# Performance work log

Hardware: AMD Instinct MI355X
Metric: run time of the kernel (lower is better)

The kernel has to match this reference:

```python
import jax, jax.numpy as jnp
import numpy as np

H = 2048            # hidden_size
INTER = 8192        # intermediate_size
E = 16              # num_experts
V = 32000           # vocab_size
I = INTER // E      # per-expert intermediate (tp_size=1) = 512
N = 4096            # num_tokens
BASE_ROUTING_SCALE = 10.0


def setup_inputs() -> dict:
    key = jax.random.key(0)
    ks = jax.random.split(key, 6)
    x = jax.random.normal(ks[0], (N, H), dtype=jnp.float32)
    token_ids = jax.random.randint(ks[1], (N,), 0, V)
    mu = jax.random.normal(ks[2], (N, H), dtype=jnp.float32)
    # kaiming-uniform-ish scaled params
    gate_up_proj = jax.random.normal(ks[3], (E, H, 2 * I), dtype=jnp.float32) * (1.0 / np.sqrt(H))
    down_proj = jax.random.normal(ks[4], (E, I, H), dtype=jnp.float32) * (1.0 / np.sqrt(I))
    # mu_router initialized to zeros in the module; use small random so routing is actually mu-biased
    mu_router_w = jax.random.normal(ks[5], (E, H), dtype=jnp.float32) * 0.02
    return {"x": x, "token_ids": token_ids, "mu": mu,
            "gate_up_proj": gate_up_proj, "down_proj": down_proj,
            "mu_router_w": mu_router_w}


def reference(x, token_ids, mu, gate_up_proj, down_proj, mu_router_w):
    # --- routing: expert = token_id % E, biased by mu logits ---
    base = jnp.clip(token_ids, 0, V - 1) % E              # [N]
    logits = (jax.nn.one_hot(base, E, dtype=jnp.float32) * BASE_ROUTING_SCALE
              + mu @ mu_router_w.T)                       # [N, E]
    expert_ids = jnp.argmax(logits, axis=-1)              # [N]

    Iloc = gate_up_proj.shape[-1] // 2

    # --- grouped expert SwiGLU MLP: scan over experts, mask-combine outputs ---
    def step(acc, inp):
        wg, wd, e = inp
        gu = x @ wg                                       # [N, 2I]
        h = jax.nn.silu(gu[:, :Iloc]) * gu[:, Iloc:]      # [N, I]
        o = h @ wd                                        # [N, H]
        acc = acc + jnp.where((expert_ids == e)[:, None], o, 0.0)
        return acc, None

    out0 = jnp.zeros_like(x)
    out, _ = jax.lax.scan(step, out0, (gate_up_proj, down_proj, jnp.arange(E)))
    return out
```

## Files before the change

### kernel.cpp

```cpp
#include <hip/hip_runtime.h>
#include <hip/hip_bf16.h>

#define NT 4096
#define HD 2048
#define NE 16
#define ID 512
#define TWO_I 1024
#define PITCH 72
#define MAXITEMS 47

typedef __attribute__((ext_vector_type(8))) short bf16x8_t;
typedef __attribute__((ext_vector_type(4))) float f32x4_t;

__device__ __forceinline__ unsigned short f2bf(float f) {
  union { float f; unsigned int u; } v; v.f = f;
  unsigned int r = v.u + 0x7fffu + ((v.u >> 16) & 1u);
  return (unsigned short)(r >> 16);
}

__global__ void k_cast_x(const float* __restrict__ x, unsigned short* __restrict__ xb) {
  size_t i = ((size_t)blockIdx.x * 256 + threadIdx.x) * 8;
  float4 a = *(const float4*)(x + i);
  float4 b = *(const float4*)(x + i + 4);
  unsigned int w0 = (unsigned)f2bf(a.x) | ((unsigned)f2bf(a.y) << 16);
  unsigned int w1 = (unsigned)f2bf(a.z) | ((unsigned)f2bf(a.w) << 16);
  unsigned int w2 = (unsigned)f2bf(b.x) | ((unsigned)f2bf(b.y) << 16);
  unsigned int w3 = (unsigned)f2bf(b.z) | ((unsigned)f2bf(b.w) << 16);
  uint4 pk; pk.x = w0; pk.y = w1; pk.z = w2; pk.w = w3;
  *(uint4*)(xb + i) = pk;
}

__global__ void k_route(const float* __restrict__ mu, const int* __restrict__ tok,
                        const float* __restrict__ wr, int* __restrict__ eid) {
  int t = blockIdx.x;
  int tid = threadIdx.x;
  float p[NE];
#pragma unroll
  for (int e = 0; e < NE; ++e) p[e] = 0.f;
  const float* m = mu + (size_t)t * HD;
  for (int h = tid; h < HD; h += 256) {
    float mv = m[h];
#pragma unroll
    for (int e = 0; e < NE; ++e) p[e] += mv * wr[e * HD + h];
  }
#pragma unroll
  for (int e = 0; e < NE; ++e) {
    float v = p[e];
#pragma unroll
    for (int s = 32; s; s >>= 1) v += __shfl_xor(v, s, 64);
    p[e] = v;
  }
  __shared__ float red[4][NE];
  int lane = tid & 63, wv = tid >> 6;
  if (lane == 0) {
#pragma unroll
    for (int e = 0; e < NE; ++e) red[wv][e] = p[e];
  }
  __syncthreads();
  if (tid == 0) {
    int tk = tok[t];
    if (tk < 0) tk = 0;
    if (tk > 31999) tk = 31999;
    int base = tk & 15;
    float best = -3.0e38f; int bi = 0;
    for (int e = 0; e < NE; ++e) {
      float v = red[0][e] + red[1][e] + red[2][e] + red[3][e];
      if (e == base) v += 10.0f;
      if (v > best) { best = v; bi = e; }
    }
    eid[t] = bi;
  }
}

__global__ void k_init(int* counts, int* cursors) {
  int i = threadIdx.x;
  if (i < NE) { counts[i] = 0; cursors[i] = 0; }
}
__global__ void k_hist(const int* __restrict__ eid, int* __restrict__ counts) {
  int t = blockIdx.x * 256 + threadIdx.x;
  if (t < NT) atomicAdd(&counts[eid[t]], 1);
}
__global__ void k_scan(const int* __restrict__ counts, int* __restrict__ offsets,
                       int* __restrict__ cursors, int* __restrict__ wk) {
  if (threadIdx.x == 0) {
    int s = 0;
    for (int e = 0; e < NE; ++e) { offsets[e] = s; cursors[e] = s; s += counts[e]; }
    offsets[NE] = s;
    int n = 0;
    for (int e = 0; e < NE; ++e) {
      int tiles = (counts[e] + 127) >> 7;
      for (int m = 0; m < tiles; ++m) { wk[n++] = e | (m << 8); }
    }
    wk[MAXITEMS] = n;
  }
}
__global__ void k_scatter(const int* __restrict__ eid, int* __restrict__ cursors,
                          int* __restrict__ tlist) {
  int t = blockIdx.x * 256 + threadIdx.x;
  if (t < NT) {
    int e = eid[t];
    int pos = atomicAdd(&cursors[e], 1);
    tlist[pos] = t;
  }
}

__global__ __launch_bounds__(256, 3) void k_gemm1(
    const unsigned short* __restrict__ xb, const float* __restrict__ gup,
    const int* __restrict__ offsets, const int* __restrict__ tlist,
    const int* __restrict__ wk, unsigned short* __restrict__ hbuf) {
  int item = blockIdx.y;
  if (item >= wk[MAXITEMS]) return;
  int w = wk[item];
  int e = w & 255, tb = (w >> 8) * 128;
  int off = offsets[e], cnt = offsets[e + 1] - off;
  int c0 = blockIdx.x * 32;

  __shared__ unsigned short lA[128 * PITCH];
  __shared__ unsigned short lB[64 * PITCH];
  __shared__ int ltok[128];

  int tid = threadIdx.x, lane = tid & 63, wv = tid >> 6;
  if (tid < 128) {
    int r = tb + tid; if (r > cnt - 1) r = cnt - 1;
    ltok[tid] = tlist[off + r];
  }
  __syncthreads();

  const float* Wg = gup + (size_t)e * HD * TWO_I;

  const unsigned short* aP[4];
  unsigned aL[4];
#pragma unroll
  for (int it = 0; it < 4; ++it) {
    int id = tid + 256 * it;
    int row = id >> 3, oct = id & 7;
    aP[it] = xb + (size_t)ltok[row] * HD + oct * 8;
    aL[it] = row * PITCH + oct * 8;
  }
  const float* bP[2];
  unsigned bL[2];
#pragma unroll
  for (int it = 0; it < 2; ++it) {
    int id = tid + 256 * it;
    int col = id & 31, grp = (id >> 5) & 1, koct = id >> 6;
    int gcol = grp ? (ID + c0 + col) : (c0 + col);
    bP[it] = Wg + (size_t)koct * 8 * TWO_I + gcol;
    bL[it] = (grp * 32 + col) * PITCH + koct * 8;
  }

  f32x4_t zero = {0.f, 0.f, 0.f, 0.f};
  f32x4_t accg[2][2], accu[2][2];
#pragma unroll
  for (int m = 0; m < 2; ++m)
#pragma unroll
    for (int n = 0; n < 2; ++n) { accg[m][n] = zero; accu[m][n] = zero; }

  for (int kt = 0; kt < 32; ++kt) {
    uint4 a0 = *(const uint4*)aP[0], a1 = *(const uint4*)aP[1];
    uint4 a2 = *(const uint4*)aP[2], a3 = *(const uint4*)aP[3];
    float b0[8], b1[8];
#pragma unroll
    for (int j = 0; j < 8; ++j) b0[j] = bP[0][(size_t)j * TWO_I];
#pragma unroll
    for (int j = 0; j < 8; ++j) b1[j] = bP[1][(size_t)j * TWO_I];
#pragma unroll
    for (int it = 0; it < 4; ++it) aP[it] += 64;
#pragma unroll
    for (int it = 0; it < 2; ++it) bP[it] += (size_t)64 * TWO_I;

    __syncthreads();
    *(uint4*)&lA[aL[0]] = a0; *(uint4*)&lA[aL[1]] = a1;
    *(uint4*)&lA[aL[2]] = a2; *(uint4*)&lA[aL[3]] = a3;
    uint4 p0, p1;
    p0.x = (unsigned)f2bf(b0[0]) | ((unsigned)f2bf(b0[1]) << 16);
    p0.y = (unsigned)f2bf(b0[2]) | ((unsigned)f2bf(b0[3]) << 16);
    p0.z = (unsigned)f2bf(b0[4]) | ((unsigned)f2bf(b0[5]) << 16);
    p0.w = (unsigned)f2bf(b0[6]) | ((unsigned)f2bf(b0[7]) << 16);
    p1.x = (unsigned)f2bf(b1[0]) | ((unsigned)f2bf(b1[1]) << 16);
    p1.y = (unsigned)f2bf(b1[2]) | ((unsigned)f2bf(b1[3]) << 16);
    p1.z = (unsigned)f2bf(b1[4]) | ((unsigned)f2bf(b1[5]) << 16);
    p1.w = (unsigned)f2bf(b1[6]) | ((unsigned)f2bf(b1[7]) << 16);
    *(uint4*)&lB[bL[0]] = p0; *(uint4*)&lB[bL[1]] = p1;
    __syncthreads();

    int mb = wv * 32, lr = lane & 15;
#pragma unroll
    for (int kk = 0; kk < 2; ++kk) {
      int klo = kk * 32 + 8 * (lane >> 4);
      bf16x8_t a[2], bg[2], bu[2];
#pragma unroll
      for (int m = 0; m < 2; ++m) a[m] = *(bf16x8_t*)&lA[(mb + m * 16 + lr) * PITCH + klo];
#pragma unroll
      for (int n = 0; n < 2; ++n) {
        bg[n] = *(bf16x8_t*)&lB[(n * 16 + lr) * PITCH + klo];
        bu[n] = *(bf16x8_t*)&lB[((32 + n * 16) + lr) * PITCH + klo];
      }
#pragma unroll
      for (int m = 0; m < 2; ++m)
#pragma unroll
        for (int n = 0; n < 2; ++n) {
          accg[m][n] = __builtin_amdgcn_mfma_f32_16x16x32_bf16(a[m], bg[n], accg[m][n], 0, 0, 0);
          accu[m][n] = __builtin_amdgcn_mfma_f32_16x16x32_bf16(a[m], bu[n], accu[m][n], 0, 0, 0);
        }
    }
  }

  int mb = wv * 32, lr = lane & 15, rq = (lane >> 4) * 4;
#pragma unroll
  for (int m = 0; m < 2; ++m)
#pragma unroll
    for (int n = 0; n < 2; ++n)
#pragma unroll
      for (int j = 0; j < 4; ++j) {
        int r = tb + mb + m * 16 + rq + j;
        if (r < cnt) {
          float g = accg[m][n][j], u = accu[m][n][j];
          float hv = (g / (1.f + __expf(-g))) * u;
          hbuf[(size_t)(off + r) * ID + c0 + n * 16 + lr] = f2bf(hv);
        }
      }
}

__global__ __launch_bounds__(256, 3) void k_gemm2(
    const unsigned short* __restrict__ hbuf, const float* __restrict__ dwn,
    const int* __restrict__ offsets, const int* __restrict__ tlist,
    const int* __restrict__ wk, float* __restrict__ out) {
  int item = blockIdx.y;
  if (item >= wk[MAXITEMS]) return;
  int w = wk[item];
  int e = w & 255, tb = (w >> 8) * 128;
  int off = offsets[e], cnt = offsets[e + 1] - off;
  int c0 = blockIdx.x * 64;

  __shared__ unsigned short lA[128 * PITCH];
  __shared__ unsigned short lB[64 * PITCH];

  int tid = threadIdx.x, lane = tid & 63, wv = tid >> 6;

  const float* Wd = dwn + (size_t)e * ID * HD;

  const unsigned short* aP[4];
  unsigned aL[4];
#pragma unroll
  for (int it = 0; it < 4; ++it) {
    int id = tid + 256 * it;
    int row = id >> 3, oct = id & 7;
    int r = tb + row; if (r > cnt - 1) r = cnt - 1;
    aP[it] = hbuf + (size_t)(off + r) * ID + oct * 8;
    aL[it] = row * PITCH + oct * 8;
  }
  const float* bP[2];
  unsigned bL[2];
#pragma unroll
  for (int it = 0; it < 2; ++it) {
    int id = tid + 256 * it;
    int col = id & 63, koct = id >> 6;
    bP[it] = Wd + (size_t)koct * 8 * HD + c0 + col;
    bL[it] = col * PITCH + koct * 8;
  }

  f32x4_t zero = {0.f, 0.f, 0.f, 0.f};
  f32x4_t acc[2][4];
#pragma unroll
  for (int m = 0; m < 2; ++m)
#pragma unroll
    for (int n = 0; n < 4; ++n) acc[m][n] = zero;

  for (int kt = 0; kt < 8; ++kt) {
    uint4 a0 = *(const uint4*)aP[0], a1 = *(const uint4*)aP[1];
    uint4 a2 = *(const uint4*)aP[2], a3 = *(const uint4*)aP[3];
    float b0[8], b1[8];
#pragma unroll
    for (int j = 0; j < 8; ++j) b0[j] = bP[0][(size_t)j * HD];
#pragma unroll
    for (int j = 0; j < 8; ++j) b1[j] = bP[1][(size_t)j * HD];
#pragma unroll
    for (int it = 0; it < 4; ++it) aP[it] += 64;
#pragma unroll
    for (int it = 0; it < 2; ++it) bP[it] += (size_t)64 * HD;

    __syncthreads();
    *(uint4*)&lA[aL[0]] = a0; *(uint4*)&lA[aL[1]] = a1;
    *(uint4*)&lA[aL[2]] = a2; *(uint4*)&lA[aL[3]] = a3;
    uint4 p0, p1;
    p0.x = (unsigned)f2bf(b0[0]) | ((unsigned)f2bf(b0[1]) << 16);
    p0.y = (unsigned)f2bf(b0[2]) | ((unsigned)f2bf(b0[3]) << 16);
    p0.z = (unsigned)f2bf(b0[4]) | ((unsigned)f2bf(b0[5]) << 16);
    p0.w = (unsigned)f2bf(b0[6]) | ((unsigned)f2bf(b0[7]) << 16);
    p1.x = (unsigned)f2bf(b1[0]) | ((unsigned)f2bf(b1[1]) << 16);
    p1.y = (unsigned)f2bf(b1[2]) | ((unsigned)f2bf(b1[3]) << 16);
    p1.z = (unsigned)f2bf(b1[4]) | ((unsigned)f2bf(b1[5]) << 16);
    p1.w = (unsigned)f2bf(b1[6]) | ((unsigned)f2bf(b1[7]) << 16);
    *(uint4*)&lB[bL[0]] = p0; *(uint4*)&lB[bL[1]] = p1;
    __syncthreads();

    int mb = wv * 32, lr = lane & 15;
#pragma unroll
    for (int kk = 0; kk < 2; ++kk) {
      int klo = kk * 32 + 8 * (lane >> 4);
      bf16x8_t a[2], b[4];
#pragma unroll
      for (int m = 0; m < 2; ++m) a[m] = *(bf16x8_t*)&lA[(mb + m * 16 + lr) * PITCH + klo];
#pragma unroll
      for (int n = 0; n < 4; ++n) b[n] = *(bf16x8_t*)&lB[(n * 16 + lr) * PITCH + klo];
#pragma unroll
      for (int m = 0; m < 2; ++m)
#pragma unroll
        for (int n = 0; n < 4; ++n)
          acc[m][n] = __builtin_amdgcn_mfma_f32_16x16x32_bf16(a[m], b[n], acc[m][n], 0, 0, 0);
    }
  }

  int mb = wv * 32, lr = lane & 15, rq = (lane >> 4) * 4;
#pragma unroll
  for (int m = 0; m < 2; ++m)
#pragma unroll
    for (int n = 0; n < 4; ++n)
#pragma unroll
      for (int j = 0; j < 4; ++j) {
        int r = tb + mb + m * 16 + rq + j;
        if (r < cnt) {
          out[(size_t)tlist[off + r] * HD + c0 + n * 16 + lr] = acc[m][n][j];
        }
      }
}

extern "C" void kernel_launch(void* const* d_in, const int* in_sizes, int n_in,
                              void* d_out, int out_size, void* d_ws, size_t ws_size,
                              hipStream_t stream) {
  (void)in_sizes; (void)n_in; (void)out_size; (void)ws_size;
  const float* x   = (const float*)d_in[0];
  const int*   tok = (const int*)d_in[1];
  const float* mu  = (const float*)d_in[2];
  const float* gup = (const float*)d_in[3];
  const float* dwn = (const float*)d_in[4];
  const float* wr  = (const float*)d_in[5];
  float* out = (float*)d_out;

  char* ws = (char*)d_ws;
  int* eid     = (int*)ws;
  int* tlist   = (int*)(ws + 16384);
  int* counts  = (int*)(ws + 32768);
  int* offsets = (int*)(ws + 32896);
  int* cursors = (int*)(ws + 33024);
  int* wk      = (int*)(ws + 33152);
  unsigned short* xb   = (unsigned short*)(ws + 65536);
  unsigned short* hbuf = (unsigned short*)(ws + 65536 + (size_t)NT * HD * 2);

  k_cast_x <<<4096, 256, 0, stream>>>(x, xb);
  k_route  <<<NT, 256, 0, stream>>>(mu, tok, wr, eid);
  k_init   <<<1, 64, 0, stream>>>(counts, cursors);
  k_hist   <<<16, 256, 0, stream>>>(eid, counts);
  k_scan   <<<1, 64, 0, stream>>>(counts, offsets, cursors, wk);
  k_scatter<<<16, 256, 0, stream>>>(eid, cursors, tlist);
  k_gemm1  <<<dim3(16, MAXITEMS), 256, 0, stream>>>(xb, gup, offsets, tlist, wk, hbuf);
  k_gemm2  <<<dim3(32, MAXITEMS), 256, 0, stream>>>(hbuf, dwn, offsets, tlist, wk, out);
}
```

Baseline: 188.3 us.

## Double-buffer GEMM tiles with direct global-to-LDS loads and swizzled A layout

Both expert GEMM kernels now stage A (bf16 activations) and B (fp32 weights) tiles straight from global memory into LDS using global_load_lds, double-buffered so the next K-tile is fetched while the current one is computed. The fp32 weight tile is converted to bf16 in an LDS-to-LDS pass into a padded transpose buffer, and the A tile uses an XOR swizzle instead of padding to avoid bank conflicts. This targets global-load latency and register staging in the main loop. In exchange it uses much more LDS, so launch bounds drop from 3 to 2 blocks per CU, and it adds an extra barrier and conversion pass per iteration.

```diff
diff --git a/kernel.cpp b/kernel.cpp
--- a/kernel.cpp
+++ b/kernel.cpp
@@ -17,16 +17,22 @@
   unsigned int r = v.u + 0x7fffu + ((v.u >> 16) & 1u);
   return (unsigned short)(r >> 16);
 }
+__device__ __forceinline__ unsigned pk2(unsigned short a, unsigned short b) {
+  return (unsigned)a | ((unsigned)b << 16);
+}
+__device__ __forceinline__ void gl_lds16(const void* g, void* l) {
+  __builtin_amdgcn_global_load_lds(
+      (const __attribute__((address_space(1))) unsigned int*)g,
+      (__attribute__((address_space(3))) unsigned int*)l, 16, 0, 0);
+}
 
 __global__ void k_cast_x(const float* __restrict__ x, unsigned short* __restrict__ xb) {
   size_t i = ((size_t)blockIdx.x * 256 + threadIdx.x) * 8;
   float4 a = *(const float4*)(x + i);
   float4 b = *(const float4*)(x + i + 4);
-  unsigned int w0 = (unsigned)f2bf(a.x) | ((unsigned)f2bf(a.y) << 16);
-  unsigned int w1 = (unsigned)f2bf(a.z) | ((unsigned)f2bf(a.w) << 16);
-  unsigned int w2 = (unsigned)f2bf(b.x) | ((unsigned)f2bf(b.y) << 16);
-  unsigned int w3 = (unsigned)f2bf(b.z) | ((unsigned)f2bf(b.w) << 16);
-  uint4 pk; pk.x = w0; pk.y = w1; pk.z = w2; pk.w = w3;
+  uint4 pk;
+  pk.x = pk2(f2bf(a.x), f2bf(a.y)); pk.y = pk2(f2bf(a.z), f2bf(a.w));
+  pk.z = pk2(f2bf(b.x), f2bf(b.y)); pk.w = pk2(f2bf(b.z), f2bf(b.w));
   *(uint4*)(xb + i) = pk;
 }
 
@@ -104,7 +110,7 @@
   }
 }
 
-__global__ __launch_bounds__(256, 3) void k_gemm1(
+__global__ __launch_bounds__(256, 2) void k_gemm1(
     const unsigned short* __restrict__ xb, const float* __restrict__ gup,
     const int* __restrict__ offsets, const int* __restrict__ tlist,
     const int* __restrict__ wk, unsigned short* __restrict__ hbuf) {
@@ -115,38 +121,46 @@
   int off = offsets[e], cnt = offsets[e + 1] - off;
   int c0 = blockIdx.x * 32;
 
-  __shared__ unsigned short lA[128 * PITCH];
-  __shared__ unsigned short lB[64 * PITCH];
+  __shared__ unsigned short Abuf[2][128 * 64];
+  __shared__ float Bbuf[2][64 * 64];
+  __shared__ unsigned short Pbuf[64 * PITCH];
   __shared__ int ltok[128];
 
   int tid = threadIdx.x, lane = tid & 63, wv = tid >> 6;
-  if (tid < 128) {
-    int r = tb + tid; if (r > cnt - 1) r = cnt - 1;
-    ltok[tid] = tlist[off + r];
-  }
+  if (tid < 128) { int r = tb + tid; if (r > cnt - 1) r = cnt - 1; ltok[tid] = tlist[off + r]; }
   __syncthreads();
 
-  const float* Wg = gup + (size_t)e * HD * TWO_I;
-
-  const unsigned short* aP[4];
-  unsigned aL[4];
-#pragma unroll
-  for (int it = 0; it < 4; ++it) {
-    int id = tid + 256 * it;
-    int row = id >> 3, oct = id & 7;
-    aP[it] = xb + (size_t)ltok[row] * HD + oct * 8;
-    aL[it] = row * PITCH + oct * 8;
-  }
-  const float* bP[2];
-  unsigned bL[2];
-#pragma unroll
-  for (int it = 0; it < 2; ++it) {
-    int id = tid + 256 * it;
-    int col = id & 31, grp = (id >> 5) & 1, koct = id >> 6;
-    int gcol = grp ? (ID + c0 + col) : (c0 + col);
-    bP[it] = Wg + (size_t)koct * 8 * TWO_I + gcol;
-    bL[it] = (grp * 32 + col) * PITCH + koct * 8;
-  }
+  const unsigned short* aSrc[4];
+  int aDst[4];
+  int cswz = (lane & 7) ^ ((lane >> 3) & 7);
+#pragma unroll
+  for (int i = 0; i < 4; ++i) {
+    int r = wv * 32 + i * 8 + (lane >> 3);
+    aSrc[i] = xb + (size_t)ltok[r] * HD + cswz * 8;
+    aDst[i] = (wv * 32 + i * 8) * 64;
+  }
+  const float* bSrc[4];
+  int bDst[4];
+  {
+    int cc = lane & 15;
+    int gcol = (cc < 8) ? (c0 + cc * 4) : (ID + c0 + (cc - 8) * 4);
+    const float* Wg = gup + (size_t)e * HD * TWO_I;
+#pragma unroll
+    for (int i = 0; i < 4; ++i) {
+      int kr = wv * 16 + i * 4 + (lane >> 4);
+      bSrc[i] = Wg + (size_t)kr * TWO_I + gcol;
+      bDst[i] = (wv * 16 + i * 4) * 64;
+    }
+  }
+
+  auto stage = [&](int buf) {
+#pragma unroll
+    for (int i = 0; i < 4; ++i) { gl_lds16(aSrc[i], &Abuf[buf][aDst[i]]); aSrc[i] += 64; }
+#pragma unroll
+    for (int i = 0; i < 4; ++i) { gl_lds16(bSrc[i], &Bbuf[buf][bDst[i]]); bSrc[i] += (size_t)64 * TWO_I; }
+  };
+
+  stage(0);
 
   f32x4_t zero = {0.f, 0.f, 0.f, 0.f};
   f32x4_t accg[2][2], accu[2][2];
@@ -155,45 +169,50 @@
 #pragma unroll
     for (int n = 0; n < 2; ++n) { accg[m][n] = zero; accu[m][n] = zero; }
 
+  int lr = lane & 15, hi = lane >> 4, mb = wv * 32;
+
   for (int kt = 0; kt < 32; ++kt) {
-    uint4 a0 = *(const uint4*)aP[0], a1 = *(const uint4*)aP[1];
-    uint4 a2 = *(const uint4*)aP[2], a3 = *(const uint4*)aP[3];
-    float b0[8], b1[8];
-#pragma unroll
-    for (int j = 0; j < 8; ++j) b0[j] = bP[0][(size_t)j * TWO_I];
-#pragma unroll
-    for (int j = 0; j < 8; ++j) b1[j] = bP[1][(size_t)j * TWO_I];
-#pragma unroll
-    for (int it = 0; it < 4; ++it) aP[it] += 64;
-#pragma unroll
-    for (int it = 0; it < 2; ++it) bP[it] += (size_t)64 * TWO_I;
-
-    __syncthreads();
-    *(uint4*)&lA[aL[0]] = a0; *(uint4*)&lA[aL[1]] = a1;
-    *(uint4*)&lA[aL[2]] = a2; *(uint4*)&lA[aL[3]] = a3;
-    uint4 p0, p1;
-    p0.x = (unsigned)f2bf(b0[0]) | ((unsigned)f2bf(b0[1]) << 16);
-    p0.y = (unsigned)f2bf(b0[2]) | ((unsigned)f2bf(b0[3]) << 16);
-    p0.z = (unsigned)f2bf(b0[4]) | ((unsigned)f2bf(b0[5]) << 16);
-    p0.w = (unsigned)f2bf(b0[6]) | ((unsigned)f2bf(b0[7]) << 16);
-    p1.x = (unsigned)f2bf(b1[0]) | ((unsigned)f2bf(b1[1]) << 16);
-    p1.y = (unsigned)f2bf(b1[2]) | ((unsigned)f2bf(b1[3]) << 16);
-    p1.z = (unsigned)f2bf(b1[4]) | ((unsigned)f2bf(b1[5]) << 16);
-    p1.w = (unsigned)f2bf(b1[6]) | ((unsigned)f2bf(b1[7]) << 16);
-    *(uint4*)&lB[bL[0]] = p0; *(uint4*)&lB[bL[1]] = p1;
-    __syncthreads();
-
-    int mb = wv * 32, lr = lane & 15;
+    int cur = kt & 1;
+    if (kt < 31) {
+      stage(cur ^ 1);
+      asm volatile("s_waitcnt vmcnt(8)" ::: "memory");
+    } else {
+      asm volatile("s_waitcnt vmcnt(0)" ::: "memory");
+    }
+    __builtin_amdgcn_sched_barrier(0);
+    __builtin_amdgcn_s_barrier();
+
+    {
+      int c = lane, ks = wv;
+      unsigned short tmp[16];
+#pragma unroll
+      for (int j = 0; j < 16; ++j) tmp[j] = f2bf(Bbuf[cur][(ks * 16 + j) * 64 + c]);
+      uint4 p0, p1;
+      p0.x = pk2(tmp[0], tmp[1]);   p0.y = pk2(tmp[2], tmp[3]);
+      p0.z = pk2(tmp[4], tmp[5]);   p0.w = pk2(tmp[6], tmp[7]);
+      p1.x = pk2(tmp[8], tmp[9]);   p1.y = pk2(tmp[10], tmp[11]);
+      p1.z = pk2(tmp[12], tmp[13]); p1.w = pk2(tmp[14], tmp[15]);
+      *(uint4*)&Pbuf[c * PITCH + ks * 16] = p0;
+      *(uint4*)&Pbuf[c * PITCH + ks * 16 + 8] = p1;
+    }
+    asm volatile("s_waitcnt lgkmcnt(0)" ::: "memory");
+    __builtin_amdgcn_sched_barrier(0);
+    __builtin_amdgcn_s_barrier();
+
 #pragma unroll
     for (int kk = 0; kk < 2; ++kk) {
-      int klo = kk * 32 + 8 * (lane >> 4);
+      int klo = kk * 32 + hi * 8;
       bf16x8_t a[2], bg[2], bu[2];
 #pragma unroll
-      for (int m = 0; m < 2; ++m) a[m] = *(bf16x8_t*)&lA[(mb + m * 16 + lr) * PITCH + klo];
+      for (int m = 0; m < 2; ++m) {
+        int R = mb + m * 16 + lr;
+        int ch = (kk * 4 + hi) ^ (R & 7);
+        a[m] = *(bf16x8_t*)&Abuf[cur][R * 64 + ch * 8];
+      }
 #pragma unroll
       for (int n = 0; n < 2; ++n) {
-        bg[n] = *(bf16x8_t*)&lB[(n * 16 + lr) * PITCH + klo];
-        bu[n] = *(bf16x8_t*)&lB[((32 + n * 16) + lr) * PITCH + klo];
+        bg[n] = *(bf16x8_t*)&Pbuf[(n * 16 + lr) * PITCH + klo];
+        bu[n] = *(bf16x8_t*)&Pbuf[(32 + n * 16 + lr) * PITCH + klo];
       }
 #pragma unroll
       for (int m = 0; m < 2; ++m)
@@ -203,9 +222,10 @@
           accu[m][n] = __builtin_amdgcn_mfma_f32_16x16x32_bf16(a[m], bu[n], accu[m][n], 0, 0, 0);
         }
     }
-  }
-
-  int mb = wv * 32, lr = lane & 15, rq = (lane >> 4) * 4;
+    if (kt < 31) __builtin_amdgcn_s_barrier();
+  }
+
+  int rq = hi * 4;
 #pragma unroll
   for (int m = 0; m < 2; ++m)
 #pragma unroll
@@ -221,7 +241,7 @@
       }
 }
 
-__global__ __launch_bounds__(256, 3) void k_gemm2(
+__global__ __launch_bounds__(256, 2) void k_gemm2(
     const unsigned short* __restrict__ hbuf, const float* __restrict__ dwn,
     const int* __restrict__ offsets, const int* __restrict__ tlist,
     const int* __restrict__ wk, float* __restrict__ out) {
@@ -232,32 +252,43 @@
   int off = offsets[e], cnt = offsets[e + 1] - off;
   int c0 = blockIdx.x * 64;
 
-  __shared__ unsigned short lA[128 * PITCH];
-  __shared__ unsigned short lB[64 * PITCH];
+  __shared__ unsigned short Abuf[2][128 * 64];
+  __shared__ float Bbuf[2][64 * 64];
+  __shared__ unsigned short Pbuf[64 * PITCH];
 
   int tid = threadIdx.x, lane = tid & 63, wv = tid >> 6;
 
-  const float* Wd = dwn + (size_t)e * ID * HD;
-
-  const unsigned short* aP[4];
-  unsigned aL[4];
-#pragma unroll
-  for (int it = 0; it < 4; ++it) {
-    int id = tid + 256 * it;
-    int row = id >> 3, oct = id & 7;
-    int r = tb + row; if (r > cnt - 1) r = cnt - 1;
-    aP[it] = hbuf + (size_t)(off + r) * ID + oct * 8;
-    aL[it] = row * PITCH + oct * 8;
-  }
-  const float* bP[2];
-  unsigned bL[2];
-#pragma unroll
-  for (int it = 0; it < 2; ++it) {
-    int id = tid + 256 * it;
-    int col = id & 63, koct = id >> 6;
-    bP[it] = Wd + (size_t)koct * 8 * HD + c0 + col;
-    bL[it] = col * PITCH + koct * 8;
-  }
+  const unsigned short* aSrc[4];
+  int aDst[4];
+  int cswz = (lane & 7) ^ ((lane >> 3) & 7);
+#pragma unroll
+  for (int i = 0; i < 4; ++i) {
+    int r = tb + wv * 32 + i * 8 + (lane >> 3);
+    if (r > cnt - 1) r = cnt - 1;
+    aSrc[i] = hbuf + (size_t)(off + r) * ID + cswz * 8;
+    aDst[i] = (wv * 32 + i * 8) * 64;
+  }
+  const float* bSrc[4];
+  int bDst[4];
+  {
+    int cc = lane & 15;
+    const float* Wd = dwn + (size_t)e * ID * HD;
+#pragma unroll
+    for (int i = 0; i < 4; ++i) {
+      int kr = wv * 16 + i * 4 + (lane >> 4);
+      bSrc[i] = Wd + (size_t)kr * HD + c0 + cc * 4;
+      bDst[i] = (wv * 16 + i * 4) * 64;
+    }
+  }
+
+  auto stage = [&](int buf) {
+#pragma unroll
+    for (int i = 0; i < 4; ++i) { gl_lds16(aSrc[i], &Abuf[buf][aDst[i]]); aSrc[i] += 64; }
+#pragma unroll
+    for (int i = 0; i < 4; ++i) { gl_lds16(bSrc[i], &Bbuf[buf][bDst[i]]); bSrc[i] += (size_t)64 * HD; }
+  };
+
+  stage(0);
 
   f32x4_t zero = {0.f, 0.f, 0.f, 0.f};
   f32x4_t acc[2][4];
@@ -266,52 +297,58 @@
 #pragma unroll
     for (int n = 0; n < 4; ++n) acc[m][n] = zero;
 
+  int lr = lane & 15, hi = lane >> 4, mb = wv * 32;
+
   for (int kt = 0; kt < 8; ++kt) {
-    uint4 a0 = *(const uint4*)aP[0], a1 = *(const uint4*)aP[1];
-    uint4 a2 = *(const uint4*)aP[2], a3 = *(const uint4*)aP[3];
-    float b0[8], b1[8];
-#pragma unroll
-    for (int j = 0; j < 8; ++j) b0[j] = bP[0][(size_t)j * HD];
-#pragma unroll
-    for (int j = 0; j < 8; ++j) b1[j] = bP[1][(size_t)j * HD];
-#pragma unroll
-    for (int it = 0; it < 4; ++it) aP[it] += 64;
-#pragma unroll
-    for (int it = 0; it < 2; ++it) bP[it] += (size_t)64 * HD;
-
-    __syncthreads();
-    *(uint4*)&lA[aL[0]] = a0; *(uint4*)&lA[aL[1]] = a1;
-    *(uint4*)&lA[aL[2]] = a2; *(uint4*)&lA[aL[3]] = a3;
-    uint4 p0, p1;
-    p0.x = (unsigned)f2bf(b0[0]) | ((unsigned)f2bf(b0[1]) << 16);
-    p0.y = (unsigned)f2bf(b0[2]) | ((unsigned)f2bf(b0[3]) << 16);
-    p0.z = (unsigned)f2bf(b0[4]) | ((unsigned)f2bf(b0[5]) << 16);
-    p0.w = (unsigned)f2bf(b0[6]) | ((unsigned)f2bf(b0[7]) << 16);
-    p1.x = (unsigned)f2bf(b1[0]) | ((unsigned)f2bf(b1[1]) << 16);
-    p1.y = (unsigned)f2bf(b1[2]) | ((unsigned)f2bf(b1[3]) << 16);
-    p1.z = (unsigned)f2bf(b1[4]) | ((unsigned)f2bf(b1[5]) << 16);
-    p1.w = (unsigned)f2bf(b1[6]) | ((unsigned)f2bf(b1[7]) << 16);
-    *(uint4*)&lB[bL[0]] = p0; *(uint4*)&lB[bL[1]] = p1;
-    __syncthreads();
-
-    int mb = wv * 32, lr = lane & 15;
+    int cur = kt & 1;
+    if (kt < 7) {
+      stage(cur ^ 1);
+      asm volatile("s_waitcnt vmcnt(8)" ::: "memory");
+    } else {
+      asm volatile("s_waitcnt vmcnt(0)" ::: "memory");
+    }
+    __builtin_amdgcn_sched_barrier(0);
+    __builtin_amdgcn_s_barrier();
+
+    {
+      int c = lane, ks = wv;
+      unsigned short tmp[16];
+#pragma unroll
+      for (int j = 0; j < 16; ++j) tmp[j] = f2bf(Bbuf[cur][(ks * 16 + j) * 64 + c]);
+      uint4 p0, p1;
+      p0.x = pk2(tmp[0], tmp[1]);   p0.y = pk2(tmp[2], tmp[3]);
+      p0.z = pk2(tmp[4], tmp[5]);   p0.w = pk2(tmp[6], tmp[7]);
+      p1.x = pk2(tmp[8], tmp[9]);   p1.y = pk2(tmp[10], tmp[11]);
+      p1.z = pk2(tmp[12], tmp[13]); p1.w = pk2(tmp[14], tmp[15]);
+      *(uint4*)&Pbuf[c * PITCH + ks * 16] = p0;
+      *(uint4*)&Pbuf[c * PITCH + ks * 16 + 8] = p1;
+    }
+    asm volatile("s_waitcnt lgkmcnt(0)" ::: "memory");
+    __builtin_amdgcn_sched_barrier(0);
+    __builtin_amdgcn_s_barrier();
+
 #pragma unroll
     for (int kk = 0; kk < 2; ++kk) {
-      int klo = kk * 32 + 8 * (lane >> 4);
+      int klo = kk * 32 + hi * 8;
       bf16x8_t a[2], b[4];
 #pragma unroll
-      for (int m = 0; m < 2; ++m) a[m] = *(bf16x8_t*)&lA[(mb + m * 16 + lr) * PITCH + klo];
-#pragma unroll
-      for (int n = 0; n < 4; ++n) b[n] = *(bf16x8_t*)&lB[(n * 16 + lr) * PITCH + klo];
+      for (int m = 0; m < 2; ++m) {
+        int R = mb + m * 16 + lr;
+        int ch = (kk * 4 + hi) ^ (R & 7);
+        a[m] = *(bf16x8_t*)&Abuf[cur][R * 64 + ch * 8];
+      }
+#pragma unroll
+      for (int n = 0; n < 4; ++n) b[n] = *(bf16x8_t*)&Pbuf[(n * 16 + lr) * PITCH + klo];
 #pragma unroll
       for (int m = 0; m < 2; ++m)
 #pragma unroll
         for (int n = 0; n < 4; ++n)
           acc[m][n] = __builtin_amdgcn_mfma_f32_16x16x32_bf16(a[m], b[n], acc[m][n], 0, 0, 0);
     }
-  }
-
-  int mb = wv * 32, lr = lane & 15, rq = (lane >> 4) * 4;
+    if (kt < 7) __builtin_amdgcn_s_barrier();
+  }
+
+  int rq = hi * 4;
 #pragma unroll
   for (int m = 0; m < 2; ++m)
 #pragma unroll
```

Result: slower. 220.9 us (+17.3%).
